# Performance work log

Measured on AMD Instinct MI355X. Metric: run time of the kernel, lower is better.

Reference implementation:

```python
import jax, jax.numpy as jnp
import numpy as np

B, T, S, H, D = 2, 2048, 2048, 16, 64
E = H * D  # embed_dim = 1024


def setup_inputs() -> dict:
    key = jax.random.key(0)
    k1, k2, k3, k4 = jax.random.split(key, 4)
    q = jax.random.normal(k1, (B, T, H, D), jnp.float32)
    kv = jax.random.normal(k2, (B, S, 2, H, D), jnp.float32)
    # nn.MultiheadAttention packed in-projection (xavier-ish scale) and out-projection
    in_proj_w = jax.random.normal(k3, (3 * E, E), jnp.float32) * (1.0 / np.sqrt(E)).astype(np.float32)
    in_proj_b = jnp.zeros((3 * E,), jnp.float32)
    out_proj_w = jax.random.normal(k4, (E, E), jnp.float32) * (1.0 / np.sqrt(E)).astype(np.float32)
    out_proj_b = jnp.zeros((E,), jnp.float32)
    return {"q": q, "kv": kv, "in_proj_w": in_proj_w, "in_proj_b": in_proj_b,
            "out_proj_w": out_proj_w, "out_proj_b": out_proj_b}


def reference(q, kv, in_proj_w, in_proj_b, out_proj_w, out_proj_b):
    Bq, Tq, Hh, Dd = q.shape
    Ss = kv.shape[1]
    Ee = Hh * Dd
    # flatten heads: q -> (B,T,E); kv unbinds k (two=0) and v (two=1)
    qf = q.reshape(Bq, Tq, Ee)
    kf = kv[:, :, 0].reshape(Bq, Ss, Ee)
    vf = kv[:, :, 1].reshape(Bq, Ss, Ee)
    wq, wk, wv = jnp.split(in_proj_w, 3, axis=0)
    bq, bk, bv = jnp.split(in_proj_b, 3)
    qp = (qf @ wq.T + bq).reshape(Bq, Tq, Hh, Dd).transpose(0, 2, 1, 3)  # bhtd
    kp = (kf @ wk.T + bk).reshape(Bq, Ss, Hh, Dd).transpose(0, 2, 1, 3)  # bhsd
    vp = (vf @ wv.T + bv).reshape(Bq, Ss, Hh, Dd).transpose(0, 2, 1, 3)  # bhsd
    scale = 1.0 / jnp.sqrt(jnp.asarray(Dd, qp.dtype))
    scores = jnp.einsum('bhtd,bhsd->bhts', qp, kp) * scale
    attn = jax.nn.softmax(scores, axis=-1)  # full SxS materialization, as in non-fused MHA
    ctx = jnp.einsum('bhts,bhsd->bhtd', attn, vp)
    ctx = ctx.transpose(0, 2, 1, 3).reshape(Bq, Tq, Ee)
    out = (ctx @ out_proj_w.T + out_proj_b).reshape(Bq, Tq, Hh, Dd)
    # need_weights=True default: weights averaged over heads -> (B,T,S)
    attn_weights = attn.mean(axis=1)
    return out, attn_weights
```

## Files before the change

kernel.cpp:

```cpp
#include <hip/hip_runtime.h>
#include <math.h>

#define Bb 2
#define Tt 2048
#define Ssz 2048
#define Hh 16
#define Dd 64
#define Ee 1024

#define NQ  (Bb*Tt*Ee)
#define NKV (Bb*Ssz*Ee)
#define NW  (3*Ee*Ee)
#define NWO (Ee*Ee)

#define LOG2E 1.44269504088896f

typedef __bf16 bf16x8 __attribute__((ext_vector_type(8)));
typedef float  floatx4 __attribute__((ext_vector_type(4)));
typedef short  short4_ __attribute__((ext_vector_type(4)));
typedef unsigned short u16;
typedef unsigned int   u32;

__device__ __forceinline__ u16 f2bf(float f) {
    __bf16 h = (__bf16)f;
    union { __bf16 h; u16 u; } v; v.h = h; return v.u;
}
__device__ __forceinline__ float bf2f(u16 b) {
    union { u32 u; float f; } v; v.u = ((u32)b) << 16; return v.f;
}
__device__ __forceinline__ float load_f(const void* p, int i, bool isbf) {
    if (isbf) return bf2f(((const u16*)p)[i]);
    return ((const float*)p)[i];
}
__device__ __forceinline__ u32 load2(const void* p, int i, bool isbf) {
    if (isbf) return ((const u32*)p)[i >> 1];
    float2 f = ((const float2*)p)[i >> 1];
    return (u32)f2bf(f.x) | ((u32)f2bf(f.y) << 16);
}

typedef __attribute__((address_space(1))) const unsigned int gas_u32;
typedef __attribute__((address_space(3))) unsigned int las_u32;
__device__ __forceinline__ void gl_lds16(const u16* g, u16* l) {
    __builtin_amdgcn_global_load_lds((gas_u32*)g, (las_u32*)l, 16, 0, 0);
}

__device__ __forceinline__ int swz(int k, int row) {
    return (k & ~63) | ((((k >> 3) ^ row) & 7) << 3) | (k & 7);
}

__global__ void k_detect(const u32* __restrict__ qw, int* __restrict__ flag) {
    __shared__ int cnt;
    if (threadIdx.x == 0) cnt = 0;
    __syncthreads();
    int h = 0;
    for (int i = threadIdx.x; i < 4096; i += 256) {
        u32 w = qw[i];
        u32 b = (w >> 8) & 0x7Fu;
        if ((b & 0x7Cu) == 0x3Cu) h++;
    }
    atomicAdd(&cnt, h);
    __syncthreads();
    if (threadIdx.x == 0) flag[0] = (cnt > 2048) ? 1 : 0;
}

__global__ void k_pack(const void* __restrict__ q, const void* __restrict__ kv,
                       const void* __restrict__ w_in, const void* __restrict__ b_in,
                       const void* __restrict__ w_out, const void* __restrict__ b_out,
                       const int* __restrict__ flag,
                       u32* __restrict__ qb, u32* __restrict__ kb, u32* __restrict__ vb,
                       u32* __restrict__ wb, u32* __restrict__ wob, float* __restrict__ biases) {
    bool isbf = flag[0] != 0;
    int i = (blockIdx.x * 256 + threadIdx.x) * 2;
    if (i < NQ) { int row = i >> 10, k = i & 1023;
        qb[(((size_t)row << 10) | (u32)swz(k, row)) >> 1] = load2(q, i, isbf); return; }
    i -= NQ;
    if (i < NKV) { int row = i >> 10, e = i & 1023;
        kb[(((size_t)row << 10) | (u32)swz(e, row)) >> 1] = load2(kv, row*2048 + e, isbf); return; }
    i -= NKV;
    if (i < NKV) { int row = i >> 10, e = i & 1023;
        vb[(((size_t)row << 10) | (u32)swz(e, row)) >> 1] = load2(kv, row*2048 + 1024 + e, isbf); return; }
    i -= NKV;
    if (i < NW) { int row = i >> 10, k = i & 1023;
        wb[(((size_t)row << 10) | (u32)swz(k, row)) >> 1] = load2(w_in, i, isbf); return; }
    i -= NW;
    if (i < NWO) { int row = i >> 10, k = i & 1023;
        wob[(((size_t)row << 10) | (u32)swz(k, row)) >> 1] = load2(w_out, i, isbf); return; }
    i -= NWO;
    if (i < 3072) { biases[i] = load_f(b_in, i, isbf); biases[i+1] = load_f(b_in, i+1, isbf); return; }
    i -= 3072;
    if (i < 1024) { biases[3072+i] = load_f(b_out, i, isbf); biases[3072+i+1] = load_f(b_out, i+1, isbf); }
}

__device__ __forceinline__ void gemm128_dbuf(const u16* __restrict__ Ab, const u16* __restrict__ Wb,
                                             u16* As, u16* Ws, floatx4 (&acc)[4][4], int tid) {
    int lane = tid & 63, w = tid >> 6, q = lane >> 4, ml = lane & 15;
    int mh = (w >> 1) * 64, nh = (w & 1) * 64;
    int rs = tid >> 3, cs = (tid & 7) * 8;
#pragma unroll
    for (int j = 0; j < 4; ++j) {
        gl_lds16(Ab + (size_t)(j*32 + rs) * 1024 + cs, &As[(j*32 + rs)*64 + cs]);
        gl_lds16(Wb + (size_t)(j*32 + rs) * 1024 + cs, &Ws[(j*32 + rs)*64 + cs]);
    }
    __syncthreads();
    int cur = 0;
    for (int k0 = 0; k0 < 1024; k0 += 64) {
        if (k0 + 64 < 1024) {
            int nb = (cur ^ 1) * 8192;
#pragma unroll
            for (int j = 0; j < 4; ++j) {
                gl_lds16(Ab + (size_t)(j*32 + rs) * 1024 + k0 + 64 + cs, &As[nb + (j*32 + rs)*64 + cs]);
                gl_lds16(Wb + (size_t)(j*32 + rs) * 1024 + k0 + 64 + cs, &Ws[nb + (j*32 + rs)*64 + cs]);
            }
        }
        const u16* Asc = As + cur * 8192;
        const u16* Wsc = Ws + cur * 8192;
#pragma unroll
        for (int kk = 0; kk < 2; ++kk) {
            int gs = (((kk*4 + q) ^ ml) & 7) * 8;
            bf16x8 af[4], bfv[4];
#pragma unroll
            for (int mt = 0; mt < 4; ++mt) af[mt]  = *(const bf16x8*)&Asc[(mh + mt*16 + ml)*64 + gs];
#pragma unroll
            for (int nt = 0; nt < 4; ++nt) bfv[nt] = *(const bf16x8*)&Wsc[(nh + nt*16 + ml)*64 + gs];
#pragma unroll
            for (int mt = 0; mt < 4; ++mt)
#pragma unroll
                for (int nt = 0; nt < 4; ++nt)
                    acc[mt][nt] = __builtin_amdgcn_mfma_f32_16x16x32_bf16(af[mt], bfv[nt], acc[mt][nt], 0, 0, 0);
        }
        __syncthreads();
        cur ^= 1;
    }
}

__global__ __launch_bounds__(512) void k_gemm_qkv(const u16* __restrict__ qb, const u16* __restrict__ kb,
                                                  const u16* __restrict__ vb, const u16* __restrict__ wb,
                                                  const float* __restrict__ biases,
                                                  u16* __restrict__ Qp, u16* __restrict__ Kp,
                                                  u16* __restrict__ Vt) {
    __shared__ u16 As[128 * 64];
    __shared__ u16 Ws[128 * 64];
    int flat = blockIdx.x + 8 * (blockIdx.y + 32 * blockIdx.z);
    int wg = (flat & 7) * 96 + (flat >> 3);
    int mode = wg >> 8;
    int rem = wg & 255;
    int m0 = (rem >> 3) * 128;
    int n0 = (rem & 7) * 128;
    const u16* A = ((mode == 0) ? qb : (mode == 1) ? kb : vb) + (size_t)m0 * 1024;
    const u16* W = wb + (size_t)mode * Ee * Ee + (size_t)n0 * 1024;
    const float* bias = biases + mode * 1024;
    int tid = threadIdx.x, lane = tid & 63;
    int w = tid >> 6;
    int q = lane >> 4, ml = lane & 15;
    int mh = (w >> 2) * 64;
    int nh = (w & 3) * 32;
    int rsw = tid >> 3, cs = (tid & 7) * 8;

    floatx4 acc[4][2];
#pragma unroll
    for (int a = 0; a < 4; ++a)
#pragma unroll
        for (int b2 = 0; b2 < 2; ++b2) acc[a][b2] = (floatx4){0.f, 0.f, 0.f, 0.f};

    for (int k0 = 0; k0 < 1024; k0 += 64) {
        __syncthreads();
#pragma unroll
        for (int j = 0; j < 2; ++j) {
            gl_lds16(A + (size_t)(j*64 + rsw) * 1024 + k0 + cs, &As[(j*64 + rsw)*64 + cs]);
            gl_lds16(W + (size_t)(j*64 + rsw) * 1024 + k0 + cs, &Ws[(j*64 + rsw)*64 + cs]);
        }
        __syncthreads();
#pragma unroll
        for (int kk = 0; kk < 2; ++kk) {
            int gs = (((kk*4 + q) ^ ml) & 7) * 8;
            bf16x8 af[4], bfv[2];
#pragma unroll
            for (int mt = 0; mt < 4; ++mt) af[mt]  = *(const bf16x8*)&As[(mh + mt*16 + ml)*64 + gs];
#pragma unroll
            for (int nt = 0; nt < 2; ++nt) bfv[nt] = *(const bf16x8*)&Ws[(nh + nt*16 + ml)*64 + gs];
#pragma unroll
            for (int mt = 0; mt < 4; ++mt)
#pragma unroll
                for (int nt = 0; nt < 2; ++nt)
                    acc[mt][nt] = __builtin_amdgcn_mfma_f32_16x16x32_bf16(af[mt], bfv[nt], acc[mt][nt], 0, 0, 0);
        }
    }

#pragma unroll
    for (int mt = 0; mt < 4; ++mt) {
#pragma unroll
        for (int nt = 0; nt < 2; ++nt) {
#pragma unroll
            for (int rg = 0; rg < 4; ++rg) {
                int m = m0 + mh + mt*16 + q*4 + rg;
                int n = n0 + nh + nt*16 + ml;
                float val = acc[mt][nt][rg] + bias[n];
                int b = m >> 11, t = m & 2047, hh = n >> 6, d = n & 63;
                if (mode == 0) {
                    int dsw = ((((d >> 3) ^ t) & 7) << 3) | (d & 7);
                    Qp[((size_t)(b*16 + hh) * 2048 + t) * 64 + dsw] = f2bf(val * (0.125f * LOG2E));
                } else if (mode == 1) {
                    int dsw = ((((d >> 3) ^ t) & 7) << 3) | (d & 7);
                    Kp[((size_t)(b*16 + hh) * 2048 + t) * 64 + dsw] = f2bf(val);
                } else {
                    int tsw = (t & ~63) | ((((t >> 3) ^ d) & 7) << 3)
                            | ((t & 7) ^ (((d >> 3) & 1) << 2));
                    Vt[((size_t)(b*16 + hh) * 64 + d) * 2048 + tsw] = f2bf(val);
                }
            }
        }
    }
}

__global__ __launch_bounds__(256) void k_gemm_out(const u16* __restrict__ A, const u16* __restrict__ W,
                                                  const float* __restrict__ bias, void* __restrict__ Cout,
                                                  const int* __restrict__ flag) {
    __shared__ u16 As[2 * 128 * 64];
    __shared__ u16 Ws[2 * 128 * 64];
    int flat = blockIdx.x + 8 * blockIdx.y;
    int wg = (flat & 7) * 32 + (flat >> 3);
    int m0 = (wg >> 3) * 128;
    int n0 = (wg & 7) * 128;
    int tid = threadIdx.x, lane = tid & 63;
    int w = tid >> 6, q = lane >> 4, ml = lane & 15;
    int mh = (w >> 1) * 64, nh = (w & 1) * 64;

    floatx4 acc[4][4];
#pragma unroll
    for (int a = 0; a < 4; ++a)
#pragma unroll
        for (int b2 = 0; b2 < 4; ++b2) acc[a][b2] = (floatx4){0.f, 0.f, 0.f, 0.f};

    gemm128_dbuf(A + (size_t)m0 * 1024, W + (size_t)n0 * 1024, As, Ws, acc, tid);

    bool outbf = flag[0] != 0;
#pragma unroll
    for (int mt = 0; mt < 4; ++mt) {
#pragma unroll
        for (int nt = 0; nt < 4; ++nt) {
#pragma unroll
            for (int rg = 0; rg < 4; ++rg) {
                int m = m0 + mh + mt*16 + q*4 + rg;
                int n = n0 + nh + nt*16 + ml;
                float val = acc[mt][nt][rg] + bias[n];
                if (outbf) ((u16*)Cout)[(size_t)m * 1024 + n] = f2bf(val);
                else       ((float*)Cout)[(size_t)m * 1024 + n] = val;
            }
        }
    }
}

__global__ __launch_bounds__(512) void k_flash(const u16* __restrict__ Qp, const u16* __restrict__ Kp,
                                               const u16* __restrict__ Vt, u16* __restrict__ ctx,
                                               float* __restrict__ lbuf) {
    __shared__ u16 smem[3 * 64 * 128];
    u16* Qs = smem;
    u16* KsB = smem + 8192;
    u16* VsB = smem + 16384;
    int flat = blockIdx.x + 16 * (blockIdx.y + 16 * blockIdx.z);
    int wg = (flat & 7) * 64 + (flat >> 3);
    int t0 = (wg & 15) * 128;
    int h  = (wg >> 4) & 15;
    int b  = wg >> 8;
    const u16* Qh = Qp + (size_t)(b*16 + h) * 2048 * 64;
    const u16* Kh = Kp + (size_t)(b*16 + h) * 2048 * 64;
    const u16* Vh = Vt + (size_t)(b*16 + h) * 64 * 2048;
    int tid = threadIdx.x, lane = tid & 63;
    int wv = tid >> 6, r = wv & 3, e = wv >> 2;
    int q = lane >> 4, ml = lane & 15;
    int rsw = tid >> 3, cs = (tid & 7) * 8;

#pragma unroll
    for (int j = 0; j < 2; ++j)
        gl_lds16(Qh + (size_t)(t0 + j*64 + rsw) * 64 + cs, &Qs[(j*64 + rsw)*64 + cs]);
    gl_lds16(Kh + (size_t)rsw * 64 + cs, &KsB[rsw*64 + cs]);
    gl_lds16(Vh + (size_t)rsw * 2048 + cs, &VsB[rsw*64 + cs]);
    __syncthreads();

    bf16x8 qf[2][2];
#pragma unroll
    for (int mt = 0; mt < 2; ++mt)
#pragma unroll
        for (int kk = 0; kk < 2; ++kk)
            qf[mt][kk] = *(const bf16x8*)&Qs[(r*32 + mt*16 + ml)*64 + (((kk*4 + q) ^ ml) & 7)*8];

    float lp[2] = {0.f, 0.f};
    floatx4 ct[2][4];
#pragma unroll
    for (int mt = 0; mt < 2; ++mt)
#pragma unroll
        for (int i = 0; i < 4; ++i) ct[mt][i] = (floatx4){0.f, 0.f, 0.f, 0.f};

    int cur = 0;
    for (int s0 = 0; s0 < 2048; s0 += 64) {
        if (s0 + 64 < 2048) {
            gl_lds16(Kh + (size_t)(s0 + 64 + rsw) * 64 + cs, &KsB[(cur ^ 1)*4096 + rsw*64 + cs]);
            gl_lds16(Vh + (size_t)rsw * 2048 + (s0 + 64) + cs, &VsB[(cur ^ 1)*4096 + rsw*64 + cs]);
        }
        const u16* Ksc = KsB + cur*4096;
        const u16* Vsc = VsB + cur*4096;

        floatx4 sc[2][2];
#pragma unroll
        for (int mt = 0; mt < 2; ++mt)
#pragma unroll
            for (int i = 0; i < 2; ++i) sc[mt][i] = (floatx4){0.f, 0.f, 0.f, 0.f};
#pragma unroll
        for (int kk = 0; kk < 2; ++kk) {
            int gs = (((kk*4 + q) ^ ml) & 7) * 8;
#pragma unroll
            for (int ntl = 0; ntl < 2; ++ntl) {
                bf16x8 kf = *(const bf16x8*)&Ksc[(e*32 + ntl*16 + ml)*64 + gs];
#pragma unroll
                for (int mt = 0; mt < 2; ++mt)
                    sc[mt][ntl] = __builtin_amdgcn_mfma_f32_16x16x32_bf16(kf, qf[mt][kk], sc[mt][ntl], 0, 0, 0);
            }
        }

        short4_ pa[2][2];
#pragma unroll
        for (int mt = 0; mt < 2; ++mt) {
#pragma unroll
            for (int ntl = 0; ntl < 2; ++ntl) {
#pragma unroll
                for (int rg = 0; rg < 4; ++rg) {
                    float p = __builtin_amdgcn_exp2f(sc[mt][ntl][rg]);
                    lp[mt] += p;
                    pa[mt][ntl][rg] = (short)f2bf(p);
                }
            }
        }

#pragma unroll
        for (int ksl = 0; ksl < 2; ++ksl) {
#pragma unroll
            for (int nt = 0; nt < 4; ++nt) {
                const u16* vp = &Vsc[(nt*16 + ml)*64
                                     + (((((e*2 + ksl)*2 + (q >> 1)) ^ ml) & 7) << 3)
                                     + ((q ^ (ml >> 3)) & 1)*4];
                short4_ vf = *(const short4_*)vp;
#pragma unroll
                for (int mt = 0; mt < 2; ++mt)
                    ct[mt][nt] = __builtin_amdgcn_mfma_f32_16x16x16bf16_1k(pa[mt][ksl], vf, ct[mt][nt], 0, 0, 0);
            }
        }

        __syncthreads();
        cur ^= 1;
    }

#pragma unroll
    for (int mt = 0; mt < 2; ++mt) {
        lp[mt] += __shfl_xor(lp[mt], 16);
        lp[mt] += __shfl_xor(lp[mt], 32);
    }

    float* redc = (float*)(smem + 8192);
    float* redl = (float*)smem;
    int basec = r*2048 + lane*32;
    if (e == 1) {
#pragma unroll
        for (int mt = 0; mt < 2; ++mt)
#pragma unroll
            for (int nt = 0; nt < 4; ++nt) {
                int g = mt*4 + nt;
                *(floatx4*)&redc[basec + ((g ^ (lane & 7)) << 2)] = ct[mt][nt];
            }
        redl[(r*64 + lane)*2]     = lp[0];
        redl[(r*64 + lane)*2 + 1] = lp[1];
    }
    __syncthreads();
    if (e == 0) {
#pragma unroll
        for (int mt = 0; mt < 2; ++mt)
#pragma unroll
            for (int nt = 0; nt < 4; ++nt) {
                int g = mt*4 + nt;
                ct[mt][nt] += *(const floatx4*)&redc[basec + ((g ^ (lane & 7)) << 2)];
            }
        lp[0] += redl[(r*64 + lane)*2];
        lp[1] += redl[(r*64 + lane)*2 + 1];

        if (lane < 16) {
            size_t base = (size_t)(b*16 + h) * 2048 + t0 + r*32;
#pragma unroll
            for (int mt = 0; mt < 2; ++mt) lbuf[base + mt*16 + lane] = lp[mt];
        }

#pragma unroll
        for (int mt = 0; mt < 2; ++mt) {
            float il[4];
#pragma unroll
            for (int rg = 0; rg < 4; ++rg) il[rg] = 1.f / __shfl(lp[mt], q*4 + rg);
#pragma unroll
            for (int nt = 0; nt < 4; ++nt) {
#pragma unroll
                for (int rg = 0; rg < 4; ++rg) {
                    int t = t0 + r*32 + mt*16 + q*4 + rg;
                    int c64 = nt*16 + ml;
                    int col = h*64 + (((((c64 >> 3) ^ t) & 7)) << 3) + (c64 & 7);
                    ctx[(size_t)(b*2048 + t) * 1024 + col] = f2bf(ct[mt][nt][rg] * il[rg]);
                }
            }
        }
    }
}

__global__ __launch_bounds__(512) void k_attnw(const u16* __restrict__ Qp, const u16* __restrict__ Kp,
                                               const float* __restrict__ lbuf,
                                               void* __restrict__ dout, const int* __restrict__ flag) {
    __shared__ u16 Qs[128 * 64];
    __shared__ u16 Ks[128 * 64];
    int s0 = blockIdx.x * 128;
    int t0 = blockIdx.y * 128;
    int b  = blockIdx.z;
    int tid = threadIdx.x, lane = tid & 63;
    int w = tid >> 6, q = lane >> 4, ml = lane & 15;
    int rsw = tid >> 3, cs = (tid & 7) * 8;

    floatx4 aw[8];
#pragma unroll
    for (int i = 0; i < 8; ++i) aw[i] = (floatx4){0.f, 0.f, 0.f, 0.f};

    for (int h = 0; h < 16; ++h) {
        const u16* Qh = Qp + (size_t)(b*16 + h) * 2048 * 64;
        const u16* Kh = Kp + (size_t)(b*16 + h) * 2048 * 64;
        __syncthreads();
#pragma unroll
        for (int j = 0; j < 2; ++j) {
            gl_lds16(Qh + (size_t)(t0 + j*64 + rsw) * 64 + cs, &Qs[(j*64 + rsw)*64 + cs]);
            gl_lds16(Kh + (size_t)(s0 + j*64 + rsw) * 64 + cs, &Ks[(j*64 + rsw)*64 + cs]);
        }
        __syncthreads();

        float il[4];
        size_t sb = (size_t)(b*16 + h) * 2048 + t0 + w*16 + q*4;
#pragma unroll
        for (int rg = 0; rg < 4; ++rg) il[rg] = 1.f / lbuf[sb + rg];

        floatx4 sc[8];
#pragma unroll
        for (int i = 0; i < 8; ++i) sc[i] = (floatx4){0.f, 0.f, 0.f, 0.f};
#pragma unroll
        for (int kk = 0; kk < 2; ++kk) {
            int gs = (((kk*4 + q) ^ ml) & 7) * 8;
            bf16x8 qfr = *(const bf16x8*)&Qs[(w*16 + ml)*64 + gs];
#pragma unroll
            for (int nt = 0; nt < 8; ++nt) {
                bf16x8 kfr = *(const bf16x8*)&Ks[(nt*16 + ml)*64 + gs];
                sc[nt] = __builtin_amdgcn_mfma_f32_16x16x32_bf16(qfr, kfr, sc[nt], 0, 0, 0);
            }
        }
#pragma unroll
        for (int nt = 0; nt < 8; ++nt)
#pragma unroll
            for (int rg = 0; rg < 4; ++rg)
                aw[nt][rg] += __builtin_amdgcn_exp2f(sc[nt][rg]) * il[rg];
    }

    bool outbf = flag[0] != 0;
    const size_t attn_base = (size_t)Bb * Tt * Ee;
#pragma unroll
    for (int nt = 0; nt < 8; ++nt) {
#pragma unroll
        for (int rg = 0; rg < 4; ++rg) {
            int t = t0 + w*16 + q*4 + rg;
            int s = s0 + nt*16 + ml;
            float val = aw[nt][rg] * 0.0625f;
            size_t idx = attn_base + (size_t)(b*2048 + t) * 2048 + s;
            if (outbf) ((u16*)dout)[idx] = f2bf(val);
            else       ((float*)dout)[idx] = val;
        }
    }
}

extern "C" void kernel_launch(void* const* d_in, const int* in_sizes, int n_in,
                              void* d_out, int out_size, void* d_ws, size_t ws_size,
                              hipStream_t stream) {
    const void* q     = d_in[0];
    const void* kv    = d_in[1];
    const void* w_in  = d_in[2];
    const void* b_in  = d_in[3];
    const void* w_out = d_in[4];
    const void* b_out = d_in[5];

    char* ws = (char*)d_ws;
    size_t off = 0;
    auto alloc = [&](size_t bytes) -> void* {
        void* p = ws + off;
        off += (bytes + 255) & ~(size_t)255;
        return p;
    };
    int*   flag   = (int*)alloc(256);
    u16*   qb     = (u16*)alloc((size_t)NQ * 2);
    u16*   kb     = (u16*)alloc((size_t)NKV * 2);
    u16*   vb     = (u16*)alloc((size_t)NKV * 2);
    u16*   wb     = (u16*)alloc((size_t)NW * 2);
    u16*   wob    = (u16*)alloc((size_t)NWO * 2);
    float* biases = (float*)alloc(4096 * 4);
    u16*   Qp     = (u16*)alloc((size_t)NQ * 2);
    u16*   Kp     = (u16*)alloc((size_t)NKV * 2);
    u16*   Vt     = (u16*)alloc((size_t)NKV * 2);
    u16*   ctx    = (u16*)alloc((size_t)NQ * 2);
    float* lbuf   = (float*)alloc((size_t)Bb * Hh * Tt * 4);

    k_detect<<<1, 256, 0, stream>>>((const u32*)q, flag);

    int totalPairs = (NQ + NKV + NKV + NW + NWO + 4096) / 2;
    k_pack<<<(totalPairs + 255) / 256, 256, 0, stream>>>(q, kv, w_in, b_in, w_out, b_out, flag,
                                                         (u32*)qb, (u32*)kb, (u32*)vb,
                                                         (u32*)wb, (u32*)wob, biases);

    k_gemm_qkv<<<dim3(8, 32, 3), 512, 0, stream>>>(qb, kb, vb, wb, biases, Qp, Kp, Vt);

    k_flash<<<dim3(Tt / 128, Hh, Bb), 512, 0, stream>>>(Qp, Kp, Vt, ctx, lbuf);
    k_attnw<<<dim3(Ssz / 128, Tt / 128, Bb), 512, 0, stream>>>(Qp, Kp, lbuf, d_out, flag);

    k_gemm_out<<<dim3(8, 32), 256, 0, stream>>>(ctx, wob, biases + 3072, d_out, flag);
}
```

Measured before the change: 275.2 us.

## Retile output GEMM to 64x128 blocks and remap attention-weight blocks across XCDs

The output projection GEMM now uses 64x128 tiles with 512 threads (8 waves, each computing 32x32) and single-buffered LDS, so it launches twice as many workgroups (512 instead of 256) to fill more CUs. The shared double-buffered gemm helper is removed. The attention-weights kernel gets a block index remap that spreads consecutive workgroups across the 8 XCDs for better L2 locality. Dropping the double buffering exposes global-load latency on each k step, and the smaller per-wave tile lowers MFMA reuse.

Result: no change. 271.8 us (-1.2%).

```diff
diff --git a/kernel.cpp b/kernel.cpp
--- a/kernel.cpp
+++ b/kernel.cpp
@@ -91,48 +91,6 @@
     if (i < 1024) { biases[3072+i] = load_f(b_out, i, isbf); biases[3072+i+1] = load_f(b_out, i+1, isbf); }
 }
 
-__device__ __forceinline__ void gemm128_dbuf(const u16* __restrict__ Ab, const u16* __restrict__ Wb,
-                                             u16* As, u16* Ws, floatx4 (&acc)[4][4], int tid) {
-    int lane = tid & 63, w = tid >> 6, q = lane >> 4, ml = lane & 15;
-    int mh = (w >> 1) * 64, nh = (w & 1) * 64;
-    int rs = tid >> 3, cs = (tid & 7) * 8;
-#pragma unroll
-    for (int j = 0; j < 4; ++j) {
-        gl_lds16(Ab + (size_t)(j*32 + rs) * 1024 + cs, &As[(j*32 + rs)*64 + cs]);
-        gl_lds16(Wb + (size_t)(j*32 + rs) * 1024 + cs, &Ws[(j*32 + rs)*64 + cs]);
-    }
-    __syncthreads();
-    int cur = 0;
-    for (int k0 = 0; k0 < 1024; k0 += 64) {
-        if (k0 + 64 < 1024) {
-            int nb = (cur ^ 1) * 8192;
-#pragma unroll
-            for (int j = 0; j < 4; ++j) {
-                gl_lds16(Ab + (size_t)(j*32 + rs) * 1024 + k0 + 64 + cs, &As[nb + (j*32 + rs)*64 + cs]);
-                gl_lds16(Wb + (size_t)(j*32 + rs) * 1024 + k0 + 64 + cs, &Ws[nb + (j*32 + rs)*64 + cs]);
-            }
-        }
-        const u16* Asc = As + cur * 8192;
-        const u16* Wsc = Ws + cur * 8192;
-#pragma unroll
-        for (int kk = 0; kk < 2; ++kk) {
-            int gs = (((kk*4 + q) ^ ml) & 7) * 8;
-            bf16x8 af[4], bfv[4];
-#pragma unroll
-            for (int mt = 0; mt < 4; ++mt) af[mt]  = *(const bf16x8*)&Asc[(mh + mt*16 + ml)*64 + gs];
-#pragma unroll
-            for (int nt = 0; nt < 4; ++nt) bfv[nt] = *(const bf16x8*)&Wsc[(nh + nt*16 + ml)*64 + gs];
-#pragma unroll
-            for (int mt = 0; mt < 4; ++mt)
-#pragma unroll
-                for (int nt = 0; nt < 4; ++nt)
-                    acc[mt][nt] = __builtin_amdgcn_mfma_f32_16x16x32_bf16(af[mt], bfv[nt], acc[mt][nt], 0, 0, 0);
-        }
-        __syncthreads();
-        cur ^= 1;
-    }
-}
-
 __global__ __launch_bounds__(512) void k_gemm_qkv(const u16* __restrict__ qb, const u16* __restrict__ kb,
                                                   const u16* __restrict__ vb, const u16* __restrict__ wb,
                                                   const float* __restrict__ biases,
@@ -212,32 +170,58 @@
     }
 }
 
-__global__ __launch_bounds__(256) void k_gemm_out(const u16* __restrict__ A, const u16* __restrict__ W,
+__global__ __launch_bounds__(512) void k_gemm_out(const u16* __restrict__ A, const u16* __restrict__ W,
                                                   const float* __restrict__ bias, void* __restrict__ Cout,
                                                   const int* __restrict__ flag) {
-    __shared__ u16 As[2 * 128 * 64];
-    __shared__ u16 Ws[2 * 128 * 64];
+    __shared__ u16 As[64 * 64];
+    __shared__ u16 Ws[128 * 64];
     int flat = blockIdx.x + 8 * blockIdx.y;
-    int wg = (flat & 7) * 32 + (flat >> 3);
-    int m0 = (wg >> 3) * 128;
+    int wg = (flat & 7) * 64 + (flat >> 3);
+    int m0 = (wg >> 3) * 64;
     int n0 = (wg & 7) * 128;
+    const u16* Ab = A + (size_t)m0 * 1024;
+    const u16* Wb = W + (size_t)n0 * 1024;
     int tid = threadIdx.x, lane = tid & 63;
-    int w = tid >> 6, q = lane >> 4, ml = lane & 15;
-    int mh = (w >> 1) * 64, nh = (w & 1) * 64;
-
-    floatx4 acc[4][4];
-#pragma unroll
-    for (int a = 0; a < 4; ++a)
-#pragma unroll
-        for (int b2 = 0; b2 < 4; ++b2) acc[a][b2] = (floatx4){0.f, 0.f, 0.f, 0.f};
-
-    gemm128_dbuf(A + (size_t)m0 * 1024, W + (size_t)n0 * 1024, As, Ws, acc, tid);
+    int w = tid >> 6;
+    int q = lane >> 4, ml = lane & 15;
+    int mh = (w >> 2) * 32;
+    int nh = (w & 3) * 32;
+    int rsw = tid >> 3, cs = (tid & 7) * 8;
+
+    floatx4 acc[2][2];
+#pragma unroll
+    for (int a = 0; a < 2; ++a)
+#pragma unroll
+        for (int b2 = 0; b2 < 2; ++b2) acc[a][b2] = (floatx4){0.f, 0.f, 0.f, 0.f};
+
+    for (int k0 = 0; k0 < 1024; k0 += 64) {
+        __syncthreads();
+        gl_lds16(Ab + (size_t)rsw * 1024 + k0 + cs, &As[rsw*64 + cs]);
+#pragma unroll
+        for (int j = 0; j < 2; ++j)
+            gl_lds16(Wb + (size_t)(j*64 + rsw) * 1024 + k0 + cs, &Ws[(j*64 + rsw)*64 + cs]);
+        __syncthreads();
+#pragma unroll
+        for (int kk = 0; kk < 2; ++kk) {
+            int gs = (((kk*4 + q) ^ ml) & 7) * 8;
+            bf16x8 af[2], bfv[2];
+#pragma unroll
+            for (int mt = 0; mt < 2; ++mt) af[mt]  = *(const bf16x8*)&As[(mh + mt*16 + ml)*64 + gs];
+#pragma unroll
+            for (int nt = 0; nt < 2; ++nt) bfv[nt] = *(const bf16x8*)&Ws[(nh + nt*16 + ml)*64 + gs];
+#pragma unroll
+            for (int mt = 0; mt < 2; ++mt)
+#pragma unroll
+                for (int nt = 0; nt < 2; ++nt)
+                    acc[mt][nt] = __builtin_amdgcn_mfma_f32_16x16x32_bf16(af[mt], bfv[nt], acc[mt][nt], 0, 0, 0);
+        }
+    }
 
     bool outbf = flag[0] != 0;
 #pragma unroll
-    for (int mt = 0; mt < 4; ++mt) {
-#pragma unroll
-        for (int nt = 0; nt < 4; ++nt) {
+    for (int mt = 0; mt < 2; ++mt) {
+#pragma unroll
+        for (int nt = 0; nt < 2; ++nt) {
 #pragma unroll
             for (int rg = 0; rg < 4; ++rg) {
                 int m = m0 + mh + mt*16 + q*4 + rg;
@@ -411,9 +395,11 @@
                                                void* __restrict__ dout, const int* __restrict__ flag) {
     __shared__ u16 Qs[128 * 64];
     __shared__ u16 Ks[128 * 64];
-    int s0 = blockIdx.x * 128;
-    int t0 = blockIdx.y * 128;
-    int b  = blockIdx.z;
+    int flat = blockIdx.x + 16 * (blockIdx.y + 16 * blockIdx.z);
+    int wg = (flat & 7) * 64 + (flat >> 3);
+    int s0 = (wg & 15) * 128;
+    int t0 = ((wg >> 4) & 15) * 128;
+    int b  = wg >> 8;
     int tid = threadIdx.x, lane = tid & 63;
     int w = tid >> 6, q = lane >> 4, ml = lane & 15;
     int rsw = tid >> 3, cs = (tid & 7) * 8;
@@ -516,5 +502,5 @@
     k_flash<<<dim3(Tt / 128, Hh, Bb), 512, 0, stream>>>(Qp, Kp, Vt, ctx, lbuf);
     k_attnw<<<dim3(Ssz / 128, Tt / 128, Bb), 512, 0, stream>>>(Qp, Kp, lbuf, d_out, flag);
 
-    k_gemm_out<<<dim3(8, 32), 256, 0, stream>>>(ctx, wob, biases + 3072, d_out, flag);
-}
+    k_gemm_out<<<dim3(8, 64), 512, 0, stream>>>(ctx, wob, biases + 3072, d_out, flag);
+}
```
